# Performance work log

Measured on AMD Instinct MI355X. Metric: run time of the kernel, lower is better.

Reference implementation:

```python
import jax, jax.numpy as jnp
import numpy as np
from jax import lax

B, C, H, W = 4, 64, 128, 128
O, KH, KW = 64, 3, 3
STRIDE, PAD, DIL = 1, 1, 1
KK = KH * KW


def conv2d(x, w, b, stride, pad, dil):
    y = lax.conv_general_dilated(
        x, w, window_strides=(stride, stride),
        padding=[(pad, pad), (pad, pad)], rhs_dilation=(dil, dil),
        dimension_numbers=('NCHW', 'OIHW', 'NCHW'))
    if b is not None:
        y = y + b[None, :, None, None]
    return y


def deform_conv2d(x, offset, mask, weight, stride, pad, dil):
    # x: [B,C,H,W]; offset: [B,2*KK,Ho,Wo] as (dy,dx) pairs per tap (torchvision order);
    # mask: [B,KK,Ho,Wo]; weight: [O,C,KH,KW]
    Bx, Cx, Hx, Wx = x.shape
    Ou, _, kh, kw = weight.shape
    kk = kh * kw
    Ho, Wo = offset.shape[2], offset.shape[3]
    off = offset.reshape(Bx, kk, 2, Ho, Wo)
    off_y, off_x = off[:, :, 0], off[:, :, 1]
    ky = (jnp.arange(kk) // kw).astype(x.dtype) * dil  # [KK]
    kx = (jnp.arange(kk) % kw).astype(x.dtype) * dil
    base_y = (jnp.arange(Ho).astype(x.dtype) * stride - pad)  # [Ho]
    base_x = (jnp.arange(Wo).astype(x.dtype) * stride - pad)
    py = off_y + ky[None, :, None, None] + base_y[None, None, :, None]  # [B,KK,Ho,Wo]
    px = off_x + kx[None, :, None, None] + base_x[None, None, None, :]
    y0 = jnp.floor(py).astype(jnp.int32)
    x0 = jnp.floor(px).astype(jnp.int32)
    y1, x1 = y0 + 1, x0 + 1
    wy1 = py - y0.astype(x.dtype)
    wx1 = px - x0.astype(x.dtype)
    wy0, wx0 = 1.0 - wy1, 1.0 - wx1
    x_flat = x.reshape(Bx, Cx, Hx * Wx)

    def gather(yi, xi):
        valid = ((yi >= 0) & (yi < Hx) & (xi >= 0) & (xi < Wx)).astype(x.dtype)
        idx = jnp.clip(yi, 0, Hx - 1) * Wx + jnp.clip(xi, 0, Wx - 1)  # [B,KK,Ho,Wo]
        v = jax.vmap(lambda xf, i: xf[:, i])(x_flat, idx.reshape(Bx, -1))  # [B,C,KK*Ho*Wo]
        return v.reshape(Bx, Cx, kk, Ho, Wo) * valid[:, None]

    val = (gather(y0, x0) * (wy0 * wx0)[:, None]
           + gather(y0, x1) * (wy0 * wx1)[:, None]
           + gather(y1, x0) * (wy1 * wx0)[:, None]
           + gather(y1, x1) * (wy1 * wx1)[:, None])  # [B,C,KK,Ho,Wo]
    val = val * mask[:, None]
    return jnp.einsum('bckhw,ock->bohw', val, weight.reshape(Ou, Cx, kk))


def setup_inputs() -> dict:
    key = jax.random.key(0)
    ks = jax.random.split(key, 8)
    x = jax.random.normal(ks[0], (B, C, H, W), jnp.float32)
    guide = jax.random.normal(ks[1], (B, C, H, W), jnp.float32)
    # NOTE: module inits offset/modulator convs to zero; we use small random
    # weights so the deformable sampling path is actually exercised.
    w_off = jax.random.normal(ks[2], (2 * KK, 2 * C, KH, KW), jnp.float32) * 0.01
    b_off = jax.random.normal(ks[3], (2 * KK,), jnp.float32) * 0.1
    w_mod = jax.random.normal(ks[4], (KK, 2 * C, KH, KW), jnp.float32) * 0.01
    b_mod = jax.random.normal(ks[5], (KK,), jnp.float32) * 0.1
    fan_in = C * KH * KW
    w_reg = jax.random.normal(ks[6], (O, C, KH, KW), jnp.float32) / np.sqrt(fan_in)
    return {"x": x, "guide": guide, "w_off": w_off, "b_off": b_off,
            "w_mod": w_mod, "b_mod": b_mod, "w_reg": w_reg}


def reference(x, guide, w_off, b_off, w_mod, b_mod, w_reg):
    fea = jnp.concatenate([x, guide], axis=1)  # [B,2C,H,W]
    offset = conv2d(fea, w_off, b_off, STRIDE, PAD, DIL)       # [B,2KK,Ho,Wo]
    modulator = 2.0 * jax.nn.sigmoid(conv2d(fea, w_mod, b_mod, STRIDE, PAD, DIL))
    return deform_conv2d(x, offset, modulator, w_reg, STRIDE, PAD, DIL)
```

## Files before the change

kernel.cpp:

```cpp
#include <hip/hip_runtime.h>
#include <math.h>

#define Bn   4
#define Cc   64
#define Hh   128
#define Ww   128
#define Oo   64
#define HW   16384
#define NPAR 27

#define WB2_OFF 0
#define WB_OFF  18432

typedef __attribute__((ext_vector_type(8))) short bf16x8;
typedef __attribute__((ext_vector_type(4))) short s16x4;
typedef __attribute__((ext_vector_type(4))) float f32x4;
typedef __attribute__((ext_vector_type(2), aligned(4))) float f32x2u;

__device__ __forceinline__ short f2bf(float f) {
    unsigned u = __builtin_bit_cast(unsigned, f);
    u += 0x7FFFu + ((u >> 16) & 1u);
    return (short)(u >> 16);
}

__global__ void prep_weights(const float* __restrict__ w_off,
                             const float* __restrict__ w_mod,
                             const float* __restrict__ w_reg,
                             float* __restrict__ ws) {
    int i = blockIdx.x * 256 + threadIdx.x;
    short* at2 = (short*)(ws + WB2_OFF);
    short* atd = (short*)(ws + WB_OFF);
    if (i < 36864) {
        int j = i & 7, l = (i >> 3) & 63, mt = (i >> 9) & 1, cc = (i >> 10) & 3, t = i >> 12;
        int lm = l & 15, quad = l >> 4;
        int row = mt * 16 + lm;
        int c = cc * 32 + quad * 8 + j;
        float v = 0.f;
        if (row < 18)      v = w_off[row * 1152 + c * 9 + t];
        else if (row < 27) v = w_mod[(row - 18) * 1152 + c * 9 + t];
        at2[i] = f2bf(v);
    } else if (i < 73728) {
        int e = i - 36864;
        int j = e & 7, l = (e >> 3) & 63, mt = (e >> 9) & 3, h = (e >> 11) & 1, t = e >> 12;
        int lm = l & 15, quad = l >> 4;
        int o = mt * 16 + lm;
        int c = h * 32 + quad * 8 + j;
        atd[e] = f2bf(w_reg[o * 576 + c * 9 + t]);
    }
}

#define CPSTR 136
#define DPSTR 36
#define DROWS 10

struct TapP {
    float wa0, wb0, wa1, wb1;
    int ia, ib, gx0, gx1;
    bool in;
};

__device__ __forceinline__ TapP tap_params_v(float py, float px, float m,
                                             int rb, int cb) {
    float fy = floorf(py), fx = floorf(px);
    int y0 = (int)fy, x0 = (int)fx;
    int y1 = y0 + 1;
    float wy1 = py - fy, wx1 = px - fx;
    float wy0 = 1.f - wy1, wx0 = 1.f - wx1;
    bool vy0 = (unsigned)y0 < 128u, vy1 = (unsigned)y1 < 128u;
    bool vx0 = (unsigned)x0 < 128u, vx1 = (unsigned)(x0 + 1) < 128u;
    int cy0 = min(max(y0, 0), 127), cy1 = min(max(y1, 0), 127);
    int bx2 = min(max(x0, 0), 126);
    bool sel_lo = (x0 < 0), sel_hi = (x0 > 126);
    float w00 = (vy0 && vx0) ? wy0 * wx0 * m : 0.f;
    float w01 = (vy0 && vx1) ? wy0 * wx1 * m : 0.f;
    float w10 = (vy1 && vx0) ? wy1 * wx0 * m : 0.f;
    float w11 = (vy1 && vx1) ? wy1 * wx1 * m : 0.f;
    TapP r;
    r.wa0 = sel_lo ? w01 : (sel_hi ? 0.f : w00);
    r.wb0 = sel_hi ? w00 : (sel_lo ? 0.f : w01);
    r.wa1 = sel_lo ? w11 : (sel_hi ? 0.f : w10);
    r.wb1 = sel_hi ? w10 : (sel_lo ? 0.f : w11);
    int ty0 = cy0 - rb, ty1 = cy1 - rb, tx = bx2 - cb;
    r.ia = ty0 * 24 + tx;
    r.ib = ty1 * 24 + tx;
    r.gx0 = (cy0 << 7) + bx2;
    r.gx1 = (cy1 << 7) + bx2;
    r.in = ((unsigned)ty0 <= (unsigned)(DROWS - 1)) &&
           ((unsigned)ty1 <= (unsigned)(DROWS - 1)) &&
           ((unsigned)tx <= 22u);
    return r;
}

__global__ __launch_bounds__(256, 4)
void fused_dcn(const float* __restrict__ x, const float* __restrict__ g,
               const float* __restrict__ ws_,
               const float* __restrict__ b_off, const float* __restrict__ b_mod,
               float* __restrict__ out) {
    __shared__ __align__(16) char Ubuf[144 * CPSTR * 2];
    short* Wd = (short*)Ubuf;
    float* Xw = (float*)Ubuf;

    const int tid = threadIdx.x;
    const int l = tid & 63, lm = l & 15, quad = l >> 4;
    const int w = __builtin_amdgcn_readfirstlane(tid >> 6);

    const int bid = ((blockIdx.z << 5) + blockIdx.y) * 8 + blockIdx.x;
    const int swz = ((bid & 7) << 7) | (bid >> 3);
    const int tx_ = swz & 7, ty_ = (swz >> 3) & 31, b = swz >> 8;
    const int ho0 = ty_ * 4, wo0 = tx_ * 16;

    const short* at2 = (const short*)(ws_ + WB2_OFF);
    const short* atd = (const short*)(ws_ + WB_OFF);
    const float* xb = x + ((size_t)(b * Cc) << 14);
    const float* gb = g + ((size_t)(b * Cc) << 14);

    {
        const int row_base = ho0 - 1;
        const int col_base = wo0 - 4;
        for (int s = tid; s < 1152; s += 256) {
            int pq = s >> 5, cq = s & 31;
            int r = pq / 6, c4 = (pq - r * 6) * 4;
            int row = row_base + r, col = col_base + c4;
            bool ok = ((unsigned)row < 128u) && ((unsigned)col < 128u);
            f32x4 v0, v1, v2, v3;
            {
                int ch = cq * 4;
                const float* p0 = (ch < Cc) ? (xb + ((size_t)ch << 14)) : (gb + ((size_t)(ch - Cc) << 14));
                const float* p1 = (ch + 1 < Cc) ? (xb + ((size_t)(ch + 1) << 14)) : (gb + ((size_t)(ch + 1 - Cc) << 14));
                const float* p2 = (ch + 2 < Cc) ? (xb + ((size_t)(ch + 2) << 14)) : (gb + ((size_t)(ch + 2 - Cc) << 14));
                const float* p3 = (ch + 3 < Cc) ? (xb + ((size_t)(ch + 3) << 14)) : (gb + ((size_t)(ch + 3 - Cc) << 14));
                f32x4 zz = {0.f, 0.f, 0.f, 0.f};
                size_t off = ((size_t)(row << 7) + col);
                v0 = ok ? *(const f32x4*)(p0 + off) : zz;
                v1 = ok ? *(const f32x4*)(p1 + off) : zz;
                v2 = ok ? *(const f32x4*)(p2 + off) : zz;
                v3 = ok ? *(const f32x4*)(p3 + off) : zz;
            }
#pragma unroll
            for (int p = 0; p < 4; p++) {
                s16x4 o4 = { f2bf(v0[p]), f2bf(v1[p]), f2bf(v2[p]), f2bf(v3[p]) };
                *(s16x4*)&Wd[(r * 24 + c4 + p) * CPSTR + cq * 4] = o4;
            }
        }
    }
    __syncthreads();

    f32x4 acc0 = {0.f, 0.f, 0.f, 0.f}, acc1 = {0.f, 0.f, 0.f, 0.f};
#pragma unroll
    for (int t = 0; t < 9; t++) {
        int dy = t / 3, dx = t - dy * 3;
        int pos = (w + dy) * 24 + (lm + dx + 3);
#pragma unroll
        for (int cc = 0; cc < 4; cc++) {
            bf16x8 bfr = *(const bf16x8*)&Wd[pos * CPSTR + cc * 32 + quad * 8];
            bf16x8 a0 = *(const bf16x8*)(at2 + t * 4096 + cc * 1024 + l * 8);
            bf16x8 a1 = *(const bf16x8*)(at2 + t * 4096 + cc * 1024 + 512 + l * 8);
            acc0 = __builtin_amdgcn_mfma_f32_16x16x32_bf16(a0, bfr, acc0, 0, 0, 0);
            acc1 = __builtin_amdgcn_mfma_f32_16x16x32_bf16(a1, bfr, acc1, 0, 0, 0);
        }
    }

    const int ho = ho0 + w, wo = wo0 + lm;
    float tr[8];
#pragma unroll
    for (int mt = 0; mt < 2; mt++) {
        f32x4 a = mt ? acc1 : acc0;
#pragma unroll
        for (int reg = 0; reg < 4; reg++) {
            int j = mt * 16 + quad * 4 + reg;
            float v = a[reg];
            float r = 0.f;
            if (j < 18) {
                int k = j >> 1;
                float vb = v + b_off[j];
                r = (j & 1) ? (vb + (float)(k - (k / 3) * 3 + wo - 1))
                            : (vb + (float)(k / 3 + ho - 1));
            } else if (j < 27) {
                int k = j - 18;
                r = 2.f / (1.f + __expf(-(v + b_mod[k])));
            }
            tr[mt * 4 + reg] = r;
        }
    }

    __syncthreads();

    const int rb = min(max(ho0 - 3, 0), 128 - DROWS);
    const int cb = min(max(wo0 - 4, 0), 128 - 24);

    auto STAGE = [&](int h) {
        for (int s = tid; s < DROWS * 6 * 8; s += 256) {
            int pq = s >> 3, cq = s & 7;
            int r = pq / 6, c4 = (pq - r * 6) * 4;
            size_t off = (size_t)((rb + r) << 7) + cb + c4;
            f32x4 v0 = *(const f32x4*)(xb + ((size_t)(h * 32 + cq * 4 + 0) << 14) + off);
            f32x4 v1 = *(const f32x4*)(xb + ((size_t)(h * 32 + cq * 4 + 1) << 14) + off);
            f32x4 v2 = *(const f32x4*)(xb + ((size_t)(h * 32 + cq * 4 + 2) << 14) + off);
            f32x4 v3 = *(const f32x4*)(xb + ((size_t)(h * 32 + cq * 4 + 3) << 14) + off);
#pragma unroll
            for (int p = 0; p < 4; p++) {
                f32x4 o4 = { v0[p], v1[p], v2[p], v3[p] };
                *(f32x4*)&Xw[(r * 24 + c4 + p) * DPSTR + cq * 4] = o4;
            }
        }
    };

    STAGE(0);
    __syncthreads();

    f32x4 acc[4];
#pragma unroll
    for (int mt = 0; mt < 4; mt++) acc[mt] = (f32x4){0.f, 0.f, 0.f, 0.f};

    auto T_LOOP = [&](int h) {
#pragma unroll
        for (int t = 0; t < 9; t++) {
            const int jy = 2 * t, jx = 2 * t + 1, jm = 18 + t;
            float py = __shfl(tr[(jy >> 4) * 4 + (jy & 3)], ((jy >> 2) & 3) * 16 + lm);
            float px = __shfl(tr[(jx >> 4) * 4 + (jx & 3)], ((jx >> 2) & 3) * 16 + lm);
            float m  = __shfl(tr[(jm >> 4) * 4 + (jm & 3)], ((jm >> 2) & 3) * 16 + lm);
            TapP P = tap_params_v(py, px, m, rb, cb);
            int ia = min(max(P.ia, 0), DROWS * 24 - 2);
            int ib = min(max(P.ib, 0), DROWS * 24 - 2);
            union { short s8[8]; bf16x8 v; } u;
#pragma unroll
            for (int hf = 0; hf < 2; hf++) {
                const float* pa = Xw + ia * DPSTR + quad * 8 + hf * 4;
                const float* pb = Xw + ib * DPSTR + quad * 8 + hf * 4;
                f32x4 c0 = *(const f32x4*)(pa);
                f32x4 c1 = *(const f32x4*)(pa + DPSTR);
                f32x4 c2 = *(const f32x4*)(pb);
                f32x4 c3 = *(const f32x4*)(pb + DPSTR);
                if (__builtin_expect(!P.in, 0)) {
#pragma unroll
                    for (int j = 0; j < 4; j++) {
                        int cch = h * 32 + quad * 8 + hf * 4 + j;
                        const float* xc = xb + ((size_t)cch << 14);
                        f32x2u q0 = *(const f32x2u*)(xc + P.gx0);
                        f32x2u q1 = *(const f32x2u*)(xc + P.gx1);
                        c0[j] = q0.x; c1[j] = q0.y; c2[j] = q1.x; c3[j] = q1.y;
                    }
                }
#pragma unroll
                for (int j = 0; j < 4; j++)
                    u.s8[hf * 4 + j] = f2bf(P.wa0 * c0[j] + P.wb0 * c1[j] +
                                            P.wa1 * c2[j] + P.wb1 * c3[j]);
            }
#pragma unroll
            for (int mt = 0; mt < 4; mt++) {
                bf16x8 a = *(const bf16x8*)(atd + t * 4096 + h * 2048 + mt * 512 + l * 8);
                acc[mt] = __builtin_amdgcn_mfma_f32_16x16x32_bf16(a, u.v, acc[mt], 0, 0, 0);
            }
        }
    };

    T_LOOP(0);
    __syncthreads();
    STAGE(1);
    __syncthreads();
    T_LOOP(1);

#pragma unroll
    for (int mt = 0; mt < 4; mt++) {
        float* op = out + ((size_t)(b * Oo + mt * 16 + quad * 4) << 14) + (ho << 7) + wo;
#pragma unroll
        for (int reg = 0; reg < 4; reg++)
            op[(size_t)reg << 14] = acc[mt][reg];
    }
}

extern "C" void kernel_launch(void* const* d_in, const int* in_sizes, int n_in,
                              void* d_out, int out_size, void* d_ws, size_t ws_size,
                              hipStream_t stream) {
    const float* x     = (const float*)d_in[0];
    const float* guide = (const float*)d_in[1];
    const float* w_off = (const float*)d_in[2];
    const float* b_off = (const float*)d_in[3];
    const float* w_mod = (const float*)d_in[4];
    const float* b_mod = (const float*)d_in[5];
    const float* w_reg = (const float*)d_in[6];
    float* out = (float*)d_out;
    float* ws  = (float*)d_ws;

    hipLaunchKernelGGL(prep_weights, dim3((73728 + 255) / 256), dim3(256),
                       0, stream, w_off, w_mod, w_reg, ws);
    hipLaunchKernelGGL(fused_dcn, dim3(Ww / 16, Hh / 4, Bn), dim3(256),
                       0, stream, x, guide, ws, b_off, b_mod, out);
}
```

Before: 128.6 us.

## Stage all 64 channels of x tile in fp16 LDS in one pass

Stores the staged input window as fp16 instead of fp32 so all 64 channels fit in shared memory at once. This removes the second staging pass and its two barriers, and computes tap parameters once per tap instead of once per channel half. LDS reads per bilinear sample are halved. The cost is fp16 rounding of x before the bilinear blend and fp16-to-fp32 conversions in the inner loop, which could shift accuracy.

```diff
diff --git a/kernel.cpp b/kernel.cpp
--- a/kernel.cpp
+++ b/kernel.cpp
@@ -21,6 +21,12 @@
     unsigned u = __builtin_bit_cast(unsigned, f);
     u += 0x7FFFu + ((u >> 16) & 1u);
     return (short)(u >> 16);
+}
+__device__ __forceinline__ short f2h(float f) {
+    return __builtin_bit_cast(short, (_Float16)f);
+}
+__device__ __forceinline__ float h2f(short s) {
+    return (float)__builtin_bit_cast(_Float16, s);
 }
 
 __global__ void prep_weights(const float* __restrict__ w_off,
@@ -50,7 +56,7 @@
 }
 
 #define CPSTR 136
-#define DPSTR 36
+#define XSTR  72
 #define DROWS 10
 
 struct TapP {
@@ -98,7 +104,7 @@
                float* __restrict__ out) {
     __shared__ __align__(16) char Ubuf[144 * CPSTR * 2];
     short* Wd = (short*)Ubuf;
-    float* Xw = (float*)Ubuf;
+    short* Xh = (short*)Ubuf;
 
     const int tid = threadIdx.x;
     const int l = tid & 63, lm = l & 15, quad = l >> 4;
@@ -188,63 +194,61 @@
     const int rb = min(max(ho0 - 3, 0), 128 - DROWS);
     const int cb = min(max(wo0 - 4, 0), 128 - 24);
 
-    auto STAGE = [&](int h) {
-        for (int s = tid; s < DROWS * 6 * 8; s += 256) {
-            int pq = s >> 3, cq = s & 7;
-            int r = pq / 6, c4 = (pq - r * 6) * 4;
-            size_t off = (size_t)((rb + r) << 7) + cb + c4;
-            f32x4 v0 = *(const f32x4*)(xb + ((size_t)(h * 32 + cq * 4 + 0) << 14) + off);
-            f32x4 v1 = *(const f32x4*)(xb + ((size_t)(h * 32 + cq * 4 + 1) << 14) + off);
-            f32x4 v2 = *(const f32x4*)(xb + ((size_t)(h * 32 + cq * 4 + 2) << 14) + off);
-            f32x4 v3 = *(const f32x4*)(xb + ((size_t)(h * 32 + cq * 4 + 3) << 14) + off);
-#pragma unroll
-            for (int p = 0; p < 4; p++) {
-                f32x4 o4 = { v0[p], v1[p], v2[p], v3[p] };
-                *(f32x4*)&Xw[(r * 24 + c4 + p) * DPSTR + cq * 4] = o4;
-            }
-        }
-    };
-
-    STAGE(0);
+    for (int s = tid; s < 960; s += 256) {
+        int pq = s >> 4, cq = s & 15;
+        int r = pq / 6, c4 = (pq - r * 6) * 4;
+        size_t off = (size_t)((rb + r) << 7) + cb + c4;
+        f32x4 v0 = *(const f32x4*)(xb + ((size_t)(cq * 4 + 0) << 14) + off);
+        f32x4 v1 = *(const f32x4*)(xb + ((size_t)(cq * 4 + 1) << 14) + off);
+        f32x4 v2 = *(const f32x4*)(xb + ((size_t)(cq * 4 + 2) << 14) + off);
+        f32x4 v3 = *(const f32x4*)(xb + ((size_t)(cq * 4 + 3) << 14) + off);
+#pragma unroll
+        for (int p = 0; p < 4; p++) {
+            s16x4 o4 = { f2h(v0[p]), f2h(v1[p]), f2h(v2[p]), f2h(v3[p]) };
+            *(s16x4*)&Xh[(r * 24 + c4 + p) * XSTR + cq * 4] = o4;
+        }
+    }
     __syncthreads();
 
     f32x4 acc[4];
 #pragma unroll
     for (int mt = 0; mt < 4; mt++) acc[mt] = (f32x4){0.f, 0.f, 0.f, 0.f};
 
-    auto T_LOOP = [&](int h) {
-#pragma unroll
-        for (int t = 0; t < 9; t++) {
-            const int jy = 2 * t, jx = 2 * t + 1, jm = 18 + t;
-            float py = __shfl(tr[(jy >> 4) * 4 + (jy & 3)], ((jy >> 2) & 3) * 16 + lm);
-            float px = __shfl(tr[(jx >> 4) * 4 + (jx & 3)], ((jx >> 2) & 3) * 16 + lm);
-            float m  = __shfl(tr[(jm >> 4) * 4 + (jm & 3)], ((jm >> 2) & 3) * 16 + lm);
-            TapP P = tap_params_v(py, px, m, rb, cb);
-            int ia = min(max(P.ia, 0), DROWS * 24 - 2);
-            int ib = min(max(P.ib, 0), DROWS * 24 - 2);
+#pragma unroll
+    for (int t = 0; t < 9; t++) {
+        const int jy = 2 * t, jx = 2 * t + 1, jm = 18 + t;
+        float py = __shfl(tr[(jy >> 4) * 4 + (jy & 3)], ((jy >> 2) & 3) * 16 + lm);
+        float px = __shfl(tr[(jx >> 4) * 4 + (jx & 3)], ((jx >> 2) & 3) * 16 + lm);
+        float m  = __shfl(tr[(jm >> 4) * 4 + (jm & 3)], ((jm >> 2) & 3) * 16 + lm);
+        TapP P = tap_params_v(py, px, m, rb, cb);
+        int ia = min(max(P.ia, 0), DROWS * 24 - 2);
+        int ib = min(max(P.ib, 0), DROWS * 24 - 2);
+#pragma unroll
+        for (int h = 0; h < 2; h++) {
             union { short s8[8]; bf16x8 v; } u;
 #pragma unroll
             for (int hf = 0; hf < 2; hf++) {
-                const float* pa = Xw + ia * DPSTR + quad * 8 + hf * 4;
-                const float* pb = Xw + ib * DPSTR + quad * 8 + hf * 4;
-                f32x4 c0 = *(const f32x4*)(pa);
-                f32x4 c1 = *(const f32x4*)(pa + DPSTR);
-                f32x4 c2 = *(const f32x4*)(pb);
-                f32x4 c3 = *(const f32x4*)(pb + DPSTR);
-                if (__builtin_expect(!P.in, 0)) {
-#pragma unroll
-                    for (int j = 0; j < 4; j++) {
-                        int cch = h * 32 + quad * 8 + hf * 4 + j;
-                        const float* xc = xb + ((size_t)cch << 14);
-                        f32x2u q0 = *(const f32x2u*)(xc + P.gx0);
-                        f32x2u q1 = *(const f32x2u*)(xc + P.gx1);
-                        c0[j] = q0.x; c1[j] = q0.y; c2[j] = q1.x; c3[j] = q1.y;
-                    }
+                const short* pa = Xh + ia * XSTR + h * 32 + quad * 8 + hf * 4;
+                const short* pb = Xh + ib * XSTR + h * 32 + quad * 8 + hf * 4;
+                s16x4 A0 = *(const s16x4*)(pa);
+                s16x4 A1 = *(const s16x4*)(pa + XSTR);
+                s16x4 B0 = *(const s16x4*)(pb);
+                s16x4 B1 = *(const s16x4*)(pb + XSTR);
+#pragma unroll
+                for (int j = 0; j < 4; j++)
+                    u.s8[hf * 4 + j] = f2bf(P.wa0 * h2f(A0[j]) + P.wb0 * h2f(A1[j]) +
+                                            P.wa1 * h2f(B0[j]) + P.wb1 * h2f(B1[j]));
+            }
+            if (__builtin_expect(!P.in, 0)) {
+#pragma unroll
+                for (int j = 0; j < 8; j++) {
+                    int cch = h * 32 + quad * 8 + j;
+                    const float* xc = xb + ((size_t)cch << 14);
+                    f32x2u q0 = *(const f32x2u*)(xc + P.gx0);
+                    f32x2u q1 = *(const f32x2u*)(xc + P.gx1);
+                    u.s8[j] = f2bf(P.wa0 * q0.x + P.wb0 * q0.y +
+                                   P.wa1 * q1.x + P.wb1 * q1.y);
                 }
-#pragma unroll
-                for (int j = 0; j < 4; j++)
-                    u.s8[hf * 4 + j] = f2bf(P.wa0 * c0[j] + P.wb0 * c1[j] +
-                                            P.wa1 * c2[j] + P.wb1 * c3[j]);
             }
 #pragma unroll
             for (int mt = 0; mt < 4; mt++) {
@@ -252,13 +256,7 @@
                 acc[mt] = __builtin_amdgcn_mfma_f32_16x16x32_bf16(a, u.v, acc[mt], 0, 0, 0);
             }
         }
-    };
-
-    T_LOOP(0);
-    __syncthreads();
-    STAGE(1);
-    __syncthreads();
-    T_LOOP(1);
+    }
 
 #pragma unroll
     for (int mt = 0; mt < 4; mt++) {
```

Measured after the change: 128.5 us. About the same (-0.1%).
